# Optimization experiments

Hardware: AMD Instinct MI355X
Metric: run time of the kernel (lower is better)

The kernel has to match this reference:

```python
import jax, jax.numpy as jnp
import numpy as np

B, N, C_IN, FC0, K = 16, 32768, 32, 256, 1024
CHUNK = 64  # chunk over the K=1024 attention channels to bound the [N,CHUNK,C] intermediate
BN_EPS = 1e-5


def _lengths():
    rng = np.random.default_rng(0)
    r = rng.integers(1024, 3072, size=B)
    l = (r * N) // r.sum()
    l[-1] += N - l.sum()
    assert l.min() > 0 and l.sum() == N
    return jnp.asarray(l, dtype=jnp.int32)


def setup_inputs() -> dict:
    key = jax.random.key(0)
    ks = jax.random.split(key, 16)
    f32 = jnp.float32
    x = jax.random.normal(ks[0], (N, C_IN), dtype=f32)
    # conv1d_1 (1x1 conv == per-point linear), BN1
    w1 = jax.random.normal(ks[1], (FC0, C_IN), dtype=f32) * 0.1
    b1 = jax.random.normal(ks[2], (FC0,), dtype=f32) * 0.1
    g1 = 1.0 + 0.1 * jax.random.normal(ks[3], (FC0,), dtype=f32)
    be1 = 0.1 * jax.random.normal(ks[4], (FC0,), dtype=f32)
    m1 = 0.1 * jax.random.normal(ks[5], (FC0,), dtype=f32)
    v1 = 0.5 + jax.random.uniform(ks[6], (FC0,), dtype=f32)
    # conv1d_2, BN2
    w2 = jax.random.normal(ks[7], (K, FC0), dtype=f32) * 0.05
    b2 = jax.random.normal(ks[8], (K,), dtype=f32) * 0.1
    g2 = 1.0 + 0.1 * jax.random.normal(ks[9], (K,), dtype=f32)
    be2 = 0.1 * jax.random.normal(ks[10], (K,), dtype=f32)
    m2 = 0.1 * jax.random.normal(ks[11], (K,), dtype=f32)
    v2 = 0.5 + jax.random.uniform(ks[12], (K,), dtype=f32)
    # fc_1, BN3
    fcw = jax.random.normal(ks[13], (FC0, C_IN * K), dtype=f32) * 0.01
    fcb = jax.random.normal(ks[14], (FC0,), dtype=f32) * 0.1
    kb = jax.random.split(ks[15], 4)
    g3 = 1.0 + 0.1 * jax.random.normal(kb[0], (FC0,), dtype=f32)
    be3 = 0.1 * jax.random.normal(kb[1], (FC0,), dtype=f32)
    m3 = 0.1 * jax.random.normal(kb[2], (FC0,), dtype=f32)
    v3 = 0.5 + jax.random.uniform(kb[3], (FC0,), dtype=f32)
    return dict(x=x, length=_lengths(), w1=w1, b1=b1, g1=g1, be1=be1, m1=m1, v1=v1,
                w2=w2, b2=b2, g2=g2, be2=be2, m2=m2, v2=v2,
                fcw=fcw, fcb=fcb, g3=g3, be3=be3, m3=m3, v3=v3)


def _bn(x, g, b, m, v):
    # eval-mode BatchNorm (running stats)
    return (x - m) * (g * jax.lax.rsqrt(v + BN_EPS)) + b


def _forward(x, length, w1, b1, g1, be1, m1, v1, w2, b2, g2, be2, m2, v2,
             fcw, fcb, g3, be3, m3, v3):
    # attention features: conv1x1 -> BN -> ReLU, twice  -> [N, K]
    att = jax.nn.relu(_bn(x @ w1.T + b1, g1, be1, m1, v1))
    att = jax.nn.relu(_bn(att @ w2.T + b2, g2, be2, m2, v2))

    seg = jnp.repeat(jnp.arange(B, dtype=jnp.int32), length, total_repeat_length=N)  # [N]

    # per-segment softmax over the point axis (torch F.softmax(..., dim=0))
    mx = jax.ops.segment_max(att, seg, num_segments=B)              # [B, K]
    e = jnp.exp(att - mx[seg])
    w = e / jax.ops.segment_sum(e, seg, num_segments=B)[seg]        # [N, K]

    # per-segment weighted pooling: out[b] = att_b.T @ x_b, chunked over K
    chunks = []
    for s in range(0, K, CHUNK):
        contrib = w[:, s:s + CHUNK, None] * x[:, None, :]           # [N, CHUNK, C]
        chunks.append(jax.ops.segment_sum(contrib, seg, num_segments=B))
    pooled = jnp.concatenate(chunks, axis=1)                        # [B, K, C]
    pooled = pooled / length[:, None, None].astype(x.dtype)
    out2 = pooled.reshape(B, K * C_IN)                              # row-major flatten of [K, C]

    r = _bn(out2 @ fcw.T + fcb, g3, be3, m3, v3)                    # [B, 256]
    # F.normalize(p=2, dim=1, eps=1e-12)
    return r / jnp.maximum(jnp.linalg.norm(r, axis=1, keepdims=True), 1e-12)


def reference(x, length, w1, b1, g1, be1, m1, v1, w2, b2, g2, be2, m2, v2,
              fcw, fcb, g3, be3, m3, v3):
    return _forward(x, length, w1, b1, g1, be1, m1, v1, w2, b2, g2, be2, m2, v2,
                    fcw, fcb, g3, be3, m3, v3)
```

## Files before the change

kernel.cpp:

```cpp
#include <hip/hip_runtime.h>
#include <hip/hip_bf16.h>

typedef __bf16 bf16x8 __attribute__((ext_vector_type(8)));
typedef unsigned short u16x8 __attribute__((ext_vector_type(8)));
typedef float f32x4 __attribute__((ext_vector_type(4)));
typedef unsigned long long ull;

__device__ inline unsigned short f2bf(float f) {
    unsigned u = __builtin_bit_cast(unsigned, f);
    unsigned r = (u + 0x7fffu + ((u >> 16) & 1u)) >> 16;
    return (unsigned short)r;
}
__device__ inline float bf2f(unsigned short h) {
    unsigned u = ((unsigned)h) << 16;
    return __builtin_bit_cast(float, u);
}

__device__ inline void gload_lds16(const void* g, void* l) {
    __builtin_amdgcn_global_load_lds((const __attribute__((address_space(1))) void*)g,
                                     (__attribute__((address_space(3))) void*)l, 16, 0, 0);
}

#define MAXCH 272

__global__ __launch_bounds__(256) void k01_prep_gemm1(const float* __restrict__ x,
                                                      const float* __restrict__ w1,
                                                      const float* __restrict__ b1,
                                                      const float* __restrict__ g1,
                                                      const float* __restrict__ be1,
                                                      const float* __restrict__ m1,
                                                      const float* __restrict__ v1,
                                                      const float* __restrict__ w2,
                                                      const int* __restrict__ length,
                                                      unsigned short* __restrict__ w2p,
                                                      int* __restrict__ meta,
                                                      unsigned short* __restrict__ att1) {
    int tid = threadIdx.x;
    int i = blockIdx.x * 256 + tid;
    if (i < 32768) {
        int kb = i >> 9, kk = (i >> 6) & 7, l = i & 63;
        int col = kb * 16 + (l & 15);
        int kin = kk * 32 + (l >> 4) * 8;
        unsigned short v[8];
#pragma unroll
        for (int j = 0; j < 8; j++) v[j] = f2bf(w2[(size_t)col * 256 + kin + j]);
        *(ull*)(w2p + (size_t)i * 8)     = *(ull*)&v[0];
        *(ull*)(w2p + (size_t)i * 8 + 4) = *(ull*)&v[4];
    }
    if (blockIdx.x == 0 && tid < 64) {
        int lane = tid;
        int b = lane & 15;
        int len = length[b];
        int off = 0, chbase = 0, nch = 0;
        int nchb = (len + 127) >> 7;
#pragma unroll
        for (int j = 0; j < 16; j++) {
            int lj = __shfl(len, j, 64);
            int nj = __shfl(nchb, j, 64);
            if (j < b) { off += lj; chbase += nj; }
            nch += nj;
        }
        int total = __shfl(off + len, 15, 64);
        if (lane < 16) {
            meta[b] = off;
            meta[848 + b] = chbase;
            meta[864 + b] = chbase + nchb;
            if (b == 0) { meta[16] = total; meta[17] = nch; }
            for (int t = 0; t < nchb; t++) {
                int s = off + t * 128;
                int en = off + len < s + 128 ? off + len : s + 128;
                meta[304 + chbase + t] = s;
                meta[576 + chbase + t] = en;
            }
        }
    }
    __shared__ float xs[64][33];
    int row0 = blockIdx.x * 64;
    for (int ii = tid; ii < 64 * 32; ii += 256) {
        int rr = ii >> 5, c = ii & 31;
        xs[rr][c] = x[(row0 + rr) * 32 + c];
    }
    __syncthreads();
    int j = tid;
    float w[32];
#pragma unroll
    for (int c = 0; c < 32; c++) w[c] = w1[j * 32 + c];
    float s = g1[j] * rsqrtf(v1[j] + 1e-5f);
    float bias = (b1[j] - m1[j]) * s + be1[j];
    for (int rr = 0; rr < 64; rr++) {
        float acc = 0.f;
#pragma unroll
        for (int c = 0; c < 32; c++) acc = fmaf(xs[rr][c], w[c], acc);
        float t = fmaf(acc, s, bias);
        att1[(row0 + rr) * 256 + j] = f2bf(fmaxf(t, 0.f));
    }
}

__global__ __launch_bounds__(256, 2) void k23_fused(const unsigned short* __restrict__ att1,
                                                    const unsigned short* __restrict__ w2p,
                                                    const float* __restrict__ x,
                                                    const int* __restrict__ meta,
                                                    const float* __restrict__ b2,
                                                    const float* __restrict__ g2,
                                                    const float* __restrict__ be2,
                                                    const float* __restrict__ m2,
                                                    const float* __restrict__ v2,
                                                    unsigned short* __restrict__ pP,
                                                    float* __restrict__ pS2) {
    __shared__ __align__(16) unsigned short As[2][128 * 64];
    __shared__ __align__(16) unsigned short xT[32 * 128];
    int flat = blockIdx.x;
    int xcd = flat & 7, q = flat >> 3;
    int ch = (q >> 3) * 8 + xcd;
    int kt = q & 7;
    if (ch >= meta[17]) return;
    int n0 = meta[304 + ch];
    int rows = meta[576 + ch] - n0;
    int col0 = kt * 128;
    int tid = threadIdx.x, lane = tid & 63, wave = tid >> 6;
    int lr = lane & 15, s16 = lane >> 4;
    int wr = wave >> 1, wc = wave & 1;

    auto stage = [&](int t, int buf) {
#pragma unroll
        for (int it = 0; it < 4; it++) {
            int idx = it * 256 + tid;
            int row = idx >> 3, slot = idx & 7;
            int srow = row < rows ? row : rows - 1;
            int g = slot ^ (row & 7);
            gload_lds16(att1 + (size_t)(n0 + srow) * 256 + t * 64 + g * 8,
                        (char*)As + buf * 16384 + it * 4096 + wave * 1024);
        }
    };

    int kb0 = kt * 8 + wc * 4;
    auto loadB = [&](int t, bf16x8 (&bb)[2][4]) {
#pragma unroll
        for (int kk = 0; kk < 2; kk++)
#pragma unroll
            for (int n = 0; n < 4; n++)
                bb[kk][n] = *(const bf16x8*)(const void*)(
                    w2p + (size_t)(((kb0 + n) * 8 + t * 2 + kk) * 64 + lane) * 8);
    };

    bf16x8 b0[2][4], b1[2][4];
    stage(0, 0);
    loadB(0, b0);

#pragma unroll
    for (int p = 0; p < 8; p++) {
        int nb = p * 16 + (tid >> 5) * 2;
        int c = tid & 31;
        float v0 = (nb < rows) ? x[(size_t)(n0 + nb) * 32 + c] : 0.f;
        float v1 = (nb + 1 < rows) ? x[(size_t)(n0 + nb + 1) * 32 + c] : 0.f;
        unsigned pk = ((unsigned)f2bf(v1) << 16) | f2bf(v0);
        int byte = c * 256 + ((nb * 2) ^ ((c & 15) << 4));
        *(unsigned*)((char*)xT + byte) = pk;
    }
    __syncthreads();

    f32x4 acc[4][4] = {};
#pragma unroll
    for (int t = 0; t < 4; t++) {
        if (t < 3) stage(t + 1, (t & 1) ^ 1);
        if (t == 0) loadB(1, b1);
        else if (t == 1) loadB(2, b0);
        else if (t == 2) loadB(3, b1);
        const char* Ab = (const char*)As + (t & 1) * 16384;
#pragma unroll
        for (int kk = 0; kk < 2; kk++) {
            bf16x8 a[4];
#pragma unroll
            for (int m = 0; m < 4; m++) {
                int row = wr * 64 + m * 16 + lr;
                int slot = (kk * 4 + s16) ^ (row & 7);
                a[m] = *(const bf16x8*)(const void*)(Ab + row * 128 + slot * 16);
            }
#pragma unroll
            for (int m = 0; m < 4; m++)
#pragma unroll
                for (int n = 0; n < 4; n++)
                    acc[m][n] = __builtin_amdgcn_mfma_f32_16x16x32_bf16(
                        a[m], (t & 1) ? b1[kk][n] : b0[kk][n], acc[m][n], 0, 0, 0);
        }
        __syncthreads();
    }

    char* eT = (char*)As;
    float ssum[4] = {0.f, 0.f, 0.f, 0.f};
#pragma unroll
    for (int nf = 0; nf < 4; nf++) {
        int k = wc * 64 + nf * 16 + lr;
        int kg = col0 + k;
        float sc = g2[kg] * rsqrtf(v2[kg] + 1e-5f);
        float bias = (b2[kg] - m2[kg]) * sc + be2[kg];
#pragma unroll
        for (int m = 0; m < 4; m++) {
            int nbase = wr * 64 + m * 16 + s16 * 4;
            ull pk = 0;
#pragma unroll
            for (int rg = 0; rg < 4; rg++) {
                float tt = fmaf(acc[m][nf][rg], sc, bias);
                float ev = __expf(fmaxf(tt, 0.f));
                unsigned short h = (nbase + rg < rows) ? f2bf(ev) : (unsigned short)0;
                ssum[nf] += bf2f(h);
                pk |= ((ull)h) << (16 * rg);
            }
            int byte = k * 256 + ((nbase * 2) ^ ((k & 15) << 4));
            *(ull*)(eT + byte) = pk;
        }
    }
#pragma unroll
    for (int nf = 0; nf < 4; nf++) {
        ssum[nf] += __shfl_xor(ssum[nf], 16, 64);
        ssum[nf] += __shfl_xor(ssum[nf], 32, 64);
    }
    if (s16 == 0) {
#pragma unroll
        for (int nf = 0; nf < 4; nf++)
            pS2[ch * 2048 + wr * 1024 + col0 + wc * 64 + nf * 16 + lr] = ssum[nf];
    }
    __syncthreads();

    f32x4 pacc[2][2] = {};
#pragma unroll
    for (int nc = 0; nc < 128; nc += 32) {
        bf16x8 ea[2], xb[2];
#pragma unroll
        for (int i = 0; i < 2; i++) {
            int k = (wave * 2 + i) * 16 + lr;
            int byte = k * 256 + (((nc + s16 * 8) * 2) ^ ((k & 15) << 4));
            ea[i] = *(const bf16x8*)(const void*)(eT + byte);
        }
#pragma unroll
        for (int j = 0; j < 2; j++) {
            int c = j * 16 + lr;
            int byte = c * 256 + (((nc + s16 * 8) * 2) ^ ((c & 15) << 4));
            xb[j] = *(const bf16x8*)(const void*)((const char*)xT + byte);
        }
#pragma unroll
        for (int i = 0; i < 2; i++)
#pragma unroll
            for (int j = 0; j < 2; j++)
                pacc[i][j] = __builtin_amdgcn_mfma_f32_16x16x32_bf16(ea[i], xb[j], pacc[i][j], 0, 0, 0);
    }

    unsigned short* pPc = pP + (size_t)ch * 32768;
#pragma unroll
    for (int i = 0; i < 2; i++) {
#pragma unroll
        for (int j = 0; j < 2; j++) {
            int c = j * 16 + lr;
#pragma unroll
            for (int rg = 0; rg < 4; rg++) {
                int k = (wave * 2 + i) * 16 + s16 * 4 + rg;
                pPc[(col0 + k) * 32 + c] = f2bf(pacc[i][j][rg]);
            }
        }
    }
}

__global__ __launch_bounds__(256) void k3b_reduce(const unsigned short* __restrict__ pP,
                                                  const float* __restrict__ pS2,
                                                  const int* __restrict__ meta,
                                                  float* __restrict__ out2) {
    int id = blockIdx.x * 256 + threadIdx.x;
    int base = id * 8;
    int b = base >> 15, rem = base & 32767, k = rem >> 5;
    float P[8] = {};
    float S = 0.f;
    int c0 = meta[848 + b], c1 = meta[864 + b];
    for (int ch = c0; ch < c1; ch++) {
        u16x8 v = *(const u16x8*)(const void*)(pP + (size_t)ch * 32768 + rem);
#pragma unroll
        for (int j = 0; j < 8; j++) P[j] += bf2f(v[j]);
        S += pS2[ch * 2048 + k] + pS2[ch * 2048 + 1024 + k];
    }
    float inv = 1.f / (S * (float)(meta[b + 1] - meta[b]));
    f32x4 o0 = {P[0] * inv, P[1] * inv, P[2] * inv, P[3] * inv};
    f32x4 o1 = {P[4] * inv, P[5] * inv, P[6] * inv, P[7] * inv};
    *(f32x4*)(void*)(out2 + base) = o0;
    *(f32x4*)(void*)(out2 + base + 4) = o1;
}

__global__ __launch_bounds__(256) void k4_fc(const float* __restrict__ out2,
                                             const float* __restrict__ fcw,
                                             float* __restrict__ pFC) {
    int jt = blockIdx.x, dc = blockIdx.y;
    int tid = threadIdx.x;
    float acc[16][8] = {};
#pragma unroll
    for (int i = 0; i < 16; i++) {
        int d = dc * 4096 + i * 256 + tid;
        float wv[8];
#pragma unroll
        for (int jj = 0; jj < 8; jj++) wv[jj] = fcw[(size_t)(jt * 8 + jj) * 32768 + d];
#pragma unroll
        for (int bb = 0; bb < 16; bb++) {
            float ov = out2[bb * 32768 + d];
#pragma unroll
            for (int jj = 0; jj < 8; jj++) acc[bb][jj] = fmaf(ov, wv[jj], acc[bb][jj]);
        }
    }
    __shared__ float red[32][257];
#pragma unroll
    for (int p = 0; p < 4; p++) {
#pragma unroll
        for (int q = 0; q < 4; q++)
#pragma unroll
            for (int jj = 0; jj < 8; jj++)
                red[q * 8 + jj][tid] = acc[p * 4 + q][jj];
        __syncthreads();
        int row = tid >> 3, sg = tid & 7;
        float s = 0.f;
        for (int u = sg; u < 256; u += 8) s += red[row][u];
        s += __shfl_down(s, 4, 8);
        s += __shfl_down(s, 2, 8);
        s += __shfl_down(s, 1, 8);
        if (sg == 0) {
            int bb = p * 4 + (row >> 3), jj = row & 7;
            pFC[(dc * 16 + bb) * 256 + jt * 8 + jj] = s;
        }
        __syncthreads();
    }
}

__global__ __launch_bounds__(256) void k45_fc2(const float* __restrict__ pFC,
                                               const float* __restrict__ fcb,
                                               const float* __restrict__ g3,
                                               const float* __restrict__ be3,
                                               const float* __restrict__ m3,
                                               const float* __restrict__ v3,
                                               float* __restrict__ out) {
    int b = blockIdx.x, j = threadIdx.x;
    float sum = 0.f;
#pragma unroll
    for (int dc = 0; dc < 8; dc++) sum += pFC[(dc * 16 + b) * 256 + j];
    float sc = g3[j] * rsqrtf(v3[j] + 1e-5f);
    float rv = (sum + fcb[j] - m3[j]) * sc + be3[j];
    float sq = rv * rv;
#pragma unroll
    for (int o = 32; o > 0; o >>= 1) sq += __shfl_down(sq, o, 64);
    __shared__ float wsum[4];
    if ((j & 63) == 0) wsum[j >> 6] = sq;
    __syncthreads();
    float tot = wsum[0] + wsum[1] + wsum[2] + wsum[3];
    out[b * 256 + j] = rv / fmaxf(sqrtf(tot), 1e-12f);
}

extern "C" void kernel_launch(void* const* d_in, const int* in_sizes, int n_in,
                              void* d_out, int out_size, void* d_ws, size_t ws_size,
                              hipStream_t stream) {
    const float* x    = (const float*)d_in[0];
    const int*   len  = (const int*)d_in[1];
    const float* w1   = (const float*)d_in[2];
    const float* b1   = (const float*)d_in[3];
    const float* g1   = (const float*)d_in[4];
    const float* be1  = (const float*)d_in[5];
    const float* m1   = (const float*)d_in[6];
    const float* v1   = (const float*)d_in[7];
    const float* w2   = (const float*)d_in[8];
    const float* b2   = (const float*)d_in[9];
    const float* g2   = (const float*)d_in[10];
    const float* be2  = (const float*)d_in[11];
    const float* m2   = (const float*)d_in[12];
    const float* v2   = (const float*)d_in[13];
    const float* fcw  = (const float*)d_in[14];
    const float* fcb  = (const float*)d_in[15];
    const float* g3   = (const float*)d_in[16];
    const float* be3  = (const float*)d_in[17];
    const float* m3   = (const float*)d_in[18];
    const float* v3   = (const float*)d_in[19];

    char* ws = (char*)d_ws;
    int* meta            = (int*)ws;
    unsigned short* w2p  = (unsigned short*)(ws + 4096);
    unsigned short* att1 = (unsigned short*)(ws + 528384);
    unsigned short* pP   = (unsigned short*)(ws + 17305600);
    float* pS2           = (float*)(ws + 35131392);
    float* out2          = (float*)(ws + 37359616);
    float* pFC           = (float*)(ws + 39456768);
    float* out           = (float*)d_out;

    hipLaunchKernelGGL(k01_prep_gemm1, dim3(512),   dim3(256), 0, stream,
                       x, w1, b1, g1, be1, m1, v1, w2, len, w2p, meta, att1);
    hipLaunchKernelGGL(k23_fused,  dim3(MAXCH * 8), dim3(256), 0, stream, att1, w2p, x, meta, b2, g2, be2, m2, v2, pP, pS2);
    hipLaunchKernelGGL(k3b_reduce, dim3(256),       dim3(256), 0, stream, pP, pS2, meta, out2);
    hipLaunchKernelGGL(k4_fc,      dim3(32, 8),     dim3(256), 0, stream, out2, fcw, pFC);
    hipLaunchKernelGGL(k45_fc2,    dim3(16),        dim3(256), 0, stream, pFC, fcb, g3, be3, m3, v3, out);
}
```

Baseline: 97.00 us.

## Split fused attention tiles into 64-row halves with single-shot staging and higher occupancy

The fused GEMM2/softmax/pooling kernel now handles 64-row sub-chunks instead of 128-row chunks. It doubles the grid, loads the full 256-wide att1 tile into LDS in one pass without double buffering, and raises the occupancy hint to 4 blocks per SM. The reduce kernel sums twice as many partials, and the workspace grows to hold the larger partial buffers. This trades more partial-sum traffic and repeated w2 loads for more parallelism, a smaller per-block register footprint and a simpler pipeline. An unroll pragma is also added to the first GEMM loop.

After: 106.3 us. 1.1x slower.

```diff
diff --git a/kernel.cpp b/kernel.cpp
--- a/kernel.cpp
+++ b/kernel.cpp
@@ -87,6 +87,7 @@
     for (int c = 0; c < 32; c++) w[c] = w1[j * 32 + c];
     float s = g1[j] * rsqrtf(v1[j] + 1e-5f);
     float bias = (b1[j] - m1[j]) * s + be1[j];
+#pragma unroll 4
     for (int rr = 0; rr < 64; rr++) {
         float acc = 0.f;
 #pragma unroll
@@ -96,7 +97,7 @@
     }
 }
 
-__global__ __launch_bounds__(256, 2) void k23_fused(const unsigned short* __restrict__ att1,
+__global__ __launch_bounds__(256, 4) void k23_fused(const unsigned short* __restrict__ att1,
                                                     const unsigned short* __restrict__ w2p,
                                                     const float* __restrict__ x,
                                                     const int* __restrict__ meta,
@@ -106,85 +107,67 @@
                                                     const float* __restrict__ m2,
                                                     const float* __restrict__ v2,
                                                     unsigned short* __restrict__ pP,
-                                                    float* __restrict__ pS2) {
-    __shared__ __align__(16) unsigned short As[2][128 * 64];
-    __shared__ __align__(16) unsigned short xT[32 * 128];
+                                                    float* __restrict__ pS4) {
+    __shared__ __align__(16) unsigned short As[64 * 256];
+    __shared__ __align__(16) unsigned short xT[32 * 64];
     int flat = blockIdx.x;
     int xcd = flat & 7, q = flat >> 3;
-    int ch = (q >> 3) * 8 + xcd;
-    int kt = q & 7;
+    int kt = q & 7, rgq = q >> 3;
+    int rgid = rgq * 8 + xcd;
+    int ch = rgid >> 1, sub = rgid & 1;
     if (ch >= meta[17]) return;
-    int n0 = meta[304 + ch];
+    int n0 = meta[304 + ch] + sub * 64;
     int rows = meta[576 + ch] - n0;
+    if (rows > 64) rows = 64;
     int col0 = kt * 128;
     int tid = threadIdx.x, lane = tid & 63, wave = tid >> 6;
     int lr = lane & 15, s16 = lane >> 4;
-    int wr = wave >> 1, wc = wave & 1;
-
-    auto stage = [&](int t, int buf) {
-#pragma unroll
-        for (int it = 0; it < 4; it++) {
-            int idx = it * 256 + tid;
-            int row = idx >> 3, slot = idx & 7;
-            int srow = row < rows ? row : rows - 1;
-            int g = slot ^ (row & 7);
-            gload_lds16(att1 + (size_t)(n0 + srow) * 256 + t * 64 + g * 8,
-                        (char*)As + buf * 16384 + it * 4096 + wave * 1024);
-        }
-    };
-
-    int kb0 = kt * 8 + wc * 4;
-    auto loadB = [&](int t, bf16x8 (&bb)[2][4]) {
-#pragma unroll
-        for (int kk = 0; kk < 2; kk++)
-#pragma unroll
-            for (int n = 0; n < 4; n++)
-                bb[kk][n] = *(const bf16x8*)(const void*)(
-                    w2p + (size_t)(((kb0 + n) * 8 + t * 2 + kk) * 64 + lane) * 8);
-    };
-
-    bf16x8 b0[2][4], b1[2][4];
-    stage(0, 0);
-    loadB(0, b0);
+    int wrh = wave >> 1, wc = wave & 1;
 
 #pragma unroll
     for (int p = 0; p < 8; p++) {
+        int idx = p * 256 + tid;
+        int row = idx >> 5, ps = idx & 31;
+        int sl = ps ^ (row & 31);
+        int srow = row < rows ? row : rows - 1;
+        if (srow < 0) srow = 0;
+        gload_lds16(att1 + (size_t)(n0 + srow) * 256 + sl * 8,
+                    (char*)As + p * 4096 + wave * 1024);
+    }
+#pragma unroll
+    for (int p = 0; p < 4; p++) {
         int nb = p * 16 + (tid >> 5) * 2;
         int c = tid & 31;
         float v0 = (nb < rows) ? x[(size_t)(n0 + nb) * 32 + c] : 0.f;
         float v1 = (nb + 1 < rows) ? x[(size_t)(n0 + nb + 1) * 32 + c] : 0.f;
         unsigned pk = ((unsigned)f2bf(v1) << 16) | f2bf(v0);
-        int byte = c * 256 + ((nb * 2) ^ ((c & 15) << 4));
+        int byte = c * 128 + ((nb * 2) ^ ((c & 7) << 4));
         *(unsigned*)((char*)xT + byte) = pk;
     }
     __syncthreads();
 
-    f32x4 acc[4][4] = {};
-#pragma unroll
-    for (int t = 0; t < 4; t++) {
-        if (t < 3) stage(t + 1, (t & 1) ^ 1);
-        if (t == 0) loadB(1, b1);
-        else if (t == 1) loadB(2, b0);
-        else if (t == 2) loadB(3, b1);
-        const char* Ab = (const char*)As + (t & 1) * 16384;
-#pragma unroll
-        for (int kk = 0; kk < 2; kk++) {
-            bf16x8 a[4];
-#pragma unroll
-            for (int m = 0; m < 4; m++) {
-                int row = wr * 64 + m * 16 + lr;
-                int slot = (kk * 4 + s16) ^ (row & 7);
-                a[m] = *(const bf16x8*)(const void*)(Ab + row * 128 + slot * 16);
-            }
-#pragma unroll
-            for (int m = 0; m < 4; m++)
-#pragma unroll
-                for (int n = 0; n < 4; n++)
-                    acc[m][n] = __builtin_amdgcn_mfma_f32_16x16x32_bf16(
-                        a[m], (t & 1) ? b1[kk][n] : b0[kk][n], acc[m][n], 0, 0, 0);
-        }
-        __syncthreads();
-    }
+    f32x4 acc[2][4] = {};
+    int kb0 = kt * 8 + wc * 4;
+#pragma unroll
+    for (int kk = 0; kk < 8; kk++) {
+        bf16x8 a[2], b[4];
+#pragma unroll
+        for (int n = 0; n < 4; n++)
+            b[n] = *(const bf16x8*)(const void*)(
+                w2p + (size_t)(((kb0 + n) * 8 + kk) * 64 + lane) * 8);
+#pragma unroll
+        for (int m = 0; m < 2; m++) {
+            int row = wrh * 32 + m * 16 + lr;
+            int ps = (kk * 4 + s16) ^ (row & 31);
+            a[m] = *(const bf16x8*)(const void*)((const char*)As + row * 512 + ps * 16);
+        }
+#pragma unroll
+        for (int m = 0; m < 2; m++)
+#pragma unroll
+            for (int n = 0; n < 4; n++)
+                acc[m][n] = __builtin_amdgcn_mfma_f32_16x16x32_bf16(a[m], b[n], acc[m][n], 0, 0, 0);
+    }
+    __syncthreads();
 
     char* eT = (char*)As;
     float ssum[4] = {0.f, 0.f, 0.f, 0.f};
@@ -195,18 +178,18 @@
         float sc = g2[kg] * rsqrtf(v2[kg] + 1e-5f);
         float bias = (b2[kg] - m2[kg]) * sc + be2[kg];
 #pragma unroll
-        for (int m = 0; m < 4; m++) {
-            int nbase = wr * 64 + m * 16 + s16 * 4;
+        for (int m = 0; m < 2; m++) {
+            int nbase = wrh * 32 + m * 16 + s16 * 4;
             ull pk = 0;
 #pragma unroll
-            for (int rg = 0; rg < 4; rg++) {
-                float tt = fmaf(acc[m][nf][rg], sc, bias);
+            for (int rr = 0; rr < 4; rr++) {
+                float tt = fmaf(acc[m][nf][rr], sc, bias);
                 float ev = __expf(fmaxf(tt, 0.f));
-                unsigned short h = (nbase + rg < rows) ? f2bf(ev) : (unsigned short)0;
+                unsigned short h = (nbase + rr < rows) ? f2bf(ev) : (unsigned short)0;
                 ssum[nf] += bf2f(h);
-                pk |= ((ull)h) << (16 * rg);
+                pk |= ((ull)h) << (16 * rr);
             }
-            int byte = k * 256 + ((nbase * 2) ^ ((k & 15) << 4));
+            int byte = k * 128 + ((nbase * 2) ^ ((k & 7) << 4));
             *(ull*)(eT + byte) = pk;
         }
     }
@@ -218,24 +201,25 @@
     if (s16 == 0) {
 #pragma unroll
         for (int nf = 0; nf < 4; nf++)
-            pS2[ch * 2048 + wr * 1024 + col0 + wc * 64 + nf * 16 + lr] = ssum[nf];
+            pS4[rgid * 2048 + wrh * 1024 + col0 + wc * 64 + nf * 16 + lr] = ssum[nf];
     }
     __syncthreads();
 
     f32x4 pacc[2][2] = {};
 #pragma unroll
-    for (int nc = 0; nc < 128; nc += 32) {
+    for (int qn = 0; qn < 2; qn++) {
         bf16x8 ea[2], xb[2];
+        int nq2 = (qn * 32 + s16 * 8) * 2;
 #pragma unroll
         for (int i = 0; i < 2; i++) {
             int k = (wave * 2 + i) * 16 + lr;
-            int byte = k * 256 + (((nc + s16 * 8) * 2) ^ ((k & 15) << 4));
+            int byte = k * 128 + (nq2 ^ ((k & 7) << 4));
             ea[i] = *(const bf16x8*)(const void*)(eT + byte);
         }
 #pragma unroll
         for (int j = 0; j < 2; j++) {
             int c = j * 16 + lr;
-            int byte = c * 256 + (((nc + s16 * 8) * 2) ^ ((c & 15) << 4));
+            int byte = c * 128 + (nq2 ^ ((c & 7) << 4));
             xb[j] = *(const bf16x8*)(const void*)((const char*)xT + byte);
         }
 #pragma unroll
@@ -245,23 +229,23 @@
                 pacc[i][j] = __builtin_amdgcn_mfma_f32_16x16x32_bf16(ea[i], xb[j], pacc[i][j], 0, 0, 0);
     }
 
-    unsigned short* pPc = pP + (size_t)ch * 32768;
+    unsigned short* pPc = pP + (size_t)rgid * 32768;
 #pragma unroll
     for (int i = 0; i < 2; i++) {
 #pragma unroll
         for (int j = 0; j < 2; j++) {
             int c = j * 16 + lr;
 #pragma unroll
-            for (int rg = 0; rg < 4; rg++) {
-                int k = (wave * 2 + i) * 16 + s16 * 4 + rg;
-                pPc[(col0 + k) * 32 + c] = f2bf(pacc[i][j][rg]);
+            for (int rr = 0; rr < 4; rr++) {
+                int k = (wave * 2 + i) * 16 + s16 * 4 + rr;
+                pPc[(col0 + k) * 32 + c] = f2bf(pacc[i][j][rr]);
             }
         }
     }
 }
 
 __global__ __launch_bounds__(256) void k3b_reduce(const unsigned short* __restrict__ pP,
-                                                  const float* __restrict__ pS2,
+                                                  const float* __restrict__ pS4,
                                                   const int* __restrict__ meta,
                                                   float* __restrict__ out2) {
     int id = blockIdx.x * 256 + threadIdx.x;
@@ -269,12 +253,12 @@
     int b = base >> 15, rem = base & 32767, k = rem >> 5;
     float P[8] = {};
     float S = 0.f;
-    int c0 = meta[848 + b], c1 = meta[864 + b];
-    for (int ch = c0; ch < c1; ch++) {
-        u16x8 v = *(const u16x8*)(const void*)(pP + (size_t)ch * 32768 + rem);
+    int r0 = meta[848 + b] * 2, r1 = meta[864 + b] * 2;
+    for (int g = r0; g < r1; g++) {
+        u16x8 v = *(const u16x8*)(const void*)(pP + (size_t)g * 32768 + rem);
 #pragma unroll
         for (int j = 0; j < 8; j++) P[j] += bf2f(v[j]);
-        S += pS2[ch * 2048 + k] + pS2[ch * 2048 + 1024 + k];
+        S += pS4[g * 2048 + k] + pS4[g * 2048 + 1024 + k];
     }
     float inv = 1.f / (S * (float)(meta[b + 1] - meta[b]));
     f32x4 o0 = {P[0] * inv, P[1] * inv, P[2] * inv, P[3] * inv};
@@ -377,15 +361,15 @@
     unsigned short* w2p  = (unsigned short*)(ws + 4096);
     unsigned short* att1 = (unsigned short*)(ws + 528384);
     unsigned short* pP   = (unsigned short*)(ws + 17305600);
-    float* pS2           = (float*)(ws + 35131392);
-    float* out2          = (float*)(ws + 37359616);
-    float* pFC           = (float*)(ws + 39456768);
+    float* pS4           = (float*)(ws + 52957184);
+    float* out2          = (float*)(ws + 57413632);
+    float* pFC           = (float*)(ws + 59510784);
     float* out           = (float*)d_out;
 
     hipLaunchKernelGGL(k01_prep_gemm1, dim3(512),   dim3(256), 0, stream,
                        x, w1, b1, g1, be1, m1, v1, w2, len, w2p, meta, att1);
-    hipLaunchKernelGGL(k23_fused,  dim3(MAXCH * 8), dim3(256), 0, stream, att1, w2p, x, meta, b2, g2, be2, m2, v2, pP, pS2);
-    hipLaunchKernelGGL(k3b_reduce, dim3(256),       dim3(256), 0, stream, pP, pS2, meta, out2);
+    hipLaunchKernelGGL(k23_fused,  dim3(544 * 8),   dim3(256), 0, stream, att1, w2p, x, meta, b2, g2, be2, m2, v2, pP, pS4);
+    hipLaunchKernelGGL(k3b_reduce, dim3(256),       dim3(256), 0, stream, pP, pS4, meta, out2);
     hipLaunchKernelGGL(k4_fc,      dim3(32, 8),     dim3(256), 0, stream, out2, fcw, pFC);
     hipLaunchKernelGGL(k45_fc2,    dim3(16),        dim3(256), 0, stream, pFC, fcb, g3, be3, m3, v3, out);
 }
```
